# Kernel optimization log

Measured on AMD Instinct MI355X. Metric: run time of the kernel, lower is better.

Reference implementation:

```python
import jax, jax.numpy as jnp
import numpy as np

N = 20000      # CG beads
F = 78         # n_atom_basis (forced by reshape(-1,78) + Linear(n_atom_basis,39))
NRBF = 20
CUTOFF = 21.0
L = 3          # num_conv
DEG = 16
EH = N * DEG // 2
EPS = 1e-15


def silu(x):
    return x * jax.nn.sigmoid(x)


def setup_inputs() -> dict:
    key = jax.random.key(0)
    ks = jax.random.split(key, 22)
    cg_xyz = jax.random.normal(ks[0], (N, 3), jnp.float32) * 10.0
    half = jax.random.randint(ks[1], (EH, 2), 0, N)
    # symmetric (already-directed) edge list -> make_directed is a no-op
    CG_nbr_list = jnp.concatenate([half, half[:, ::-1]], axis=0)
    H = jax.random.normal(ks[2], (N, F), jnp.float32)
    mapping = jax.random.randint(ks[3], (N,), 0, N)  # unused by forward
    s = 0.05
    p = lambda k, shape: jax.random.normal(k, shape, jnp.float32) * s
    return {
        'cg_xyz': cg_xyz, 'CG_nbr_list': CG_nbr_list, 'mapping': mapping, 'H': H,
        # message blocks (stacked over L layers): inv_dense (F->F->4F) + dist_embed dense (NRBF->4F)
        'msg_w1': p(ks[4], (L, F, F)),   'msg_b1': jnp.zeros((L, F)),
        'msg_w2': p(ks[5], (L, F, 4 * F)), 'msg_b2': jnp.zeros((L, 4 * F)),
        'rbf_w':  p(ks[6], (L, NRBF, 4 * F)), 'rbf_b': jnp.zeros((L, 4 * F)),
        # update blocks: U, V linear maps (no bias) + s_dense (2F->F->3F)
        'upd_wu': p(ks[7], (L, F, F)), 'upd_wv': p(ks[8], (L, F, F)),
        'upd_w1': p(ks[9], (L, 2 * F, F)), 'upd_b1': jnp.zeros((L, F)),
        'upd_w2': p(ks[10], (L, F, 3 * F)), 'upd_b2': jnp.zeros((L, 3 * F)),
        # final dense head: ReLU -> Linear(78,39) -> ReLU -> Linear(39,39)
        'dense_w1': p(ks[11], (F, 39)), 'dense_b1': jnp.zeros((39,)),
        'dense_w2': p(ks[12], (39, 39)), 'dense_b2': jnp.zeros((39,)),
    }


def reference(cg_xyz, CG_nbr_list, mapping, H,
              msg_w1, msg_b1, msg_w2, msg_b2, rbf_w, rbf_b,
              upd_wu, upd_wv, upd_w1, upd_b1, upd_w2, upd_b2,
              dense_w1, dense_b1, dense_w2, dense_b2):
    n_nodes = H.shape[0]
    i_idx = CG_nbr_list[:, 0]
    j_idx = CG_nbr_list[:, 1]
    # edge geometry (shared across layers)
    r_ij = cg_xyz[j_idx] - cg_xyz[i_idx]                      # (E,3)
    dist = jnp.sqrt((r_ij ** 2 + EPS).sum(-1))                # (E,)
    unit = r_ij / dist[:, None]
    n = jnp.arange(1, NRBF + 1, dtype=cg_xyz.dtype)
    rbf = jnp.sin(n * jnp.pi * dist[:, None] / CUTOFF) / dist[:, None]   # (E,NRBF)
    env = jnp.where(dist < CUTOFF, 0.5 * (jnp.cos(jnp.pi * dist / CUTOFF) + 1.0), 0.0)

    V = jnp.zeros((n_nodes, H.shape[1], 3), H.dtype)          # (N,F,3)
    for l in range(L):
        # ---- EquiMessageCross ----
        phi = silu(H @ msg_w1[l] + msg_b1[l]) @ msg_w2[l] + msg_b2[l]     # (N,4F)
        w_s = (rbf @ rbf_w[l] + rbf_b[l]) * env[:, None]                  # (E,4F)
        inv = phi[j_idx] * w_s                                            # (E,4F)
        s0, s1, s2, s3 = jnp.split(inv, 4, axis=-1)                       # each (E,F)
        vj = V[j_idx]                                                     # (E,F,3)
        vi = V[i_idx]
        dv = (s2[..., None] * unit[:, None, :]
              + s1[..., None] * vj
              + s3[..., None] * jnp.cross(vi, vj, axis=-1))               # (E,F,3)
        H = H + jax.ops.segment_sum(s0, i_idx, num_segments=n_nodes)
        V = V + jax.ops.segment_sum(dv, i_idx, num_segments=n_nodes)
        # ---- UpdateBlock (PaiNN) ----
        u_v = jnp.einsum('nfc,fg->ngc', V, upd_wu[l])
        v_v = jnp.einsum('nfc,fg->ngc', V, upd_wv[l])
        v_norm = jnp.sqrt((v_v ** 2).sum(-1) + EPS)                       # (N,F)
        a = silu(jnp.concatenate([H, v_norm], -1) @ upd_w1[l] + upd_b1[l]) @ upd_w2[l] + upd_b2[l]
        a_vv, a_sv, a_ss = jnp.split(a, 3, axis=-1)
        H = H + a_sv * (u_v * v_v).sum(-1) + a_ss
        V = V + a_vv[..., None] * u_v

    Vs = V.sum(-1).reshape(-1, 78)                                        # (N,78)
    out = jax.nn.relu(Vs)
    out = jax.nn.relu(out @ dense_w1 + dense_b1) @ dense_w2 + dense_b2    # (N,39)
    return H, out.reshape(-1, 13, 3)
```

## Files before the change

### kernel.cpp

```cpp
#include <hip/hip_runtime.h>
#include <hip/hip_bf16.h>
#include <cmath>

#define N_NODES 20000
#define FF 78
#define F3 234
#define F4 312
#define NRBF 20
#define CUTOFF 21.0f
#define NL 3
#define PI_F 3.14159265358979323846f
#define EPS_F 1e-15f
#define REC_STRIDE 24
#define CHUNK 64
#define UV_RN 16

__global__ void k_init(const float* __restrict__ Hin, float* __restrict__ Hcur,
                       float* __restrict__ VA, uint2* __restrict__ VbfU,
                       int* __restrict__ counts, int* __restrict__ cursor)
{
    int idx = blockIdx.x * blockDim.x + threadIdx.x;
    int stride = gridDim.x * blockDim.x;
    for (int i = idx; i < N_NODES * F3; i += stride) {
        VA[i] = 0.f;
        if (i < N_NODES * FF) Hcur[i] = Hin[i];
        if (i < N_NODES * 78) VbfU[i] = make_uint2(0u, 0u);
        if (i < N_NODES) { counts[i] = 0; cursor[i] = 0; }
    }
}

__global__ void k_geo(const float* __restrict__ xyz, const int* __restrict__ nbr,
                      float4* __restrict__ geo, int* __restrict__ counts, int E)
{
    int e = blockIdx.x * blockDim.x + threadIdx.x;
    if (e >= E) return;
    int i = nbr[2 * e], j = nbr[2 * e + 1];
    float rx = xyz[3 * j]     - xyz[3 * i];
    float ry = xyz[3 * j + 1] - xyz[3 * i + 1];
    float rz = xyz[3 * j + 2] - xyz[3 * i + 2];
    float d = sqrtf(rx * rx + ry * ry + rz * rz + 3.0f * EPS_F);
    geo[e] = make_float4(rx / d, ry / d, rz / d, d);
    if (d < CUTOFF) atomicAdd(&counts[i], 1);
}

__global__ __launch_bounds__(1024)
void k_scan(const int* __restrict__ counts, int* __restrict__ row_start, int n)
{
    __shared__ int s[1024];
    const int t = threadIdx.x;
    constexpr int PER = 20;
    const int base = t * PER;
    int loc[PER];
    int sum = 0;
    #pragma unroll
    for (int q = 0; q < PER; ++q) {
        int idx = base + q;
        int v = (idx < n) ? counts[idx] : 0;
        loc[q] = sum;
        sum += v;
    }
    s[t] = sum;
    __syncthreads();
    for (int off = 1; off < 1024; off <<= 1) {
        int add = (t >= off) ? s[t - off] : 0;
        __syncthreads();
        s[t] += add;
        __syncthreads();
    }
    const int excl = (t > 0) ? s[t - 1] : 0;
    #pragma unroll
    for (int q = 0; q < PER; ++q) {
        int idx = base + q;
        if (idx <= n) row_start[idx] = excl + loc[q];
    }
}

__global__ void k_fill(const float4* __restrict__ geo, const int* __restrict__ nbr,
                       const int* __restrict__ row_start, int* __restrict__ cursor,
                       int* __restrict__ edge_idx, int E)
{
    int e = blockIdx.x * blockDim.x + threadIdx.x;
    if (e >= E) return;
    if (geo[e].w < CUTOFF) {
        int i = nbr[2 * e];
        int pos = row_start[i] + atomicAdd(&cursor[i], 1);
        edge_idx[pos] = e;
    }
}

__global__ void k_edgerec(const float4* __restrict__ geo, const int* __restrict__ edge_idx,
                          const int* __restrict__ nbr, const int* __restrict__ row_start,
                          float* __restrict__ rec, int* __restrict__ jl, int E)
{
    int p = blockIdx.x * blockDim.x + threadIdx.x;
    int total = row_start[N_NODES];
    if (p >= total) return;
    int eidx = edge_idx[p];
    float4 g = geo[eidx];
    float d = g.w;
    float env = 0.5f * (cosf(PI_F * d / CUTOFF) + 1.0f);
    float* r = rec + (size_t)p * REC_STRIDE;
    #pragma unroll
    for (int k = 0; k < NRBF; ++k)
        r[k] = env * sinf((float)(k + 1) * (PI_F / CUTOFF) * d) / d;
    r[20] = env;
    r[21] = g.x; r[22] = g.y; r[23] = g.z;
    jl[p] = nbr[2 * eidx + 1];
}

template<int K1T, int K2T, int NC2, int CS2, int BF16OUT>
__global__ void k_mlp2(const float* __restrict__ X1, const float* __restrict__ X2,
                       const float* __restrict__ w1, const float* __restrict__ b1,
                       const float* __restrict__ w2, const float* __restrict__ b2,
                       void* __restrict__ Yv, int nrows)
{
    constexpr int R = 32;
    constexpr int K = K1T + K2T;
    __shared__ float sX[K * R];
    __shared__ float s2[78 * 33];
    const int r0 = blockIdx.x * R;
    const int tid = threadIdx.y * 78 + threadIdx.x;
    for (int idx = tid; idx < R * K; idx += 312) {
        int r = idx / K, k = idx - r * K;
        int row = r0 + r;
        float v = 0.f;
        if (row < nrows) {
            if constexpr (K2T == 0) v = X1[(size_t)row * K1T + k];
            else v = (k < K1T) ? X1[(size_t)row * K1T + k] : X2[(size_t)row * K2T + (k - K1T)];
        }
        sX[k * R + r] = v;
    }
    __syncthreads();
    const int rg = threadIdx.y * 8;
    {
        const int c = threadIdx.x;
        float acc[8];
        #pragma unroll
        for (int q = 0; q < 8; ++q) acc[q] = 0.f;
        for (int k = 0; k < K; ++k) {
            const float w = w1[k * 78 + c];
            #pragma unroll
            for (int q = 0; q < 8; ++q) acc[q] = fmaf(w, sX[k * R + rg + q], acc[q]);
        }
        const float bb = b1[c];
        #pragma unroll
        for (int q = 0; q < 8; ++q) {
            float y = acc[q] + bb;
            y = y / (1.f + expf(-y));
            s2[c * 33 + rg + q] = y;
        }
    }
    __syncthreads();
    {
        const int c0 = threadIdx.x * CS2;
        float acc[8][CS2];
        #pragma unroll
        for (int q = 0; q < 8; ++q)
            #pragma unroll
            for (int cc = 0; cc < CS2; ++cc) acc[q][cc] = 0.f;
        for (int k = 0; k < 78; ++k) {
            float xv[8];
            #pragma unroll
            for (int q = 0; q < 8; ++q) xv[q] = s2[k * 33 + rg + q];
            float wv[CS2];
            #pragma unroll
            for (int cc = 0; cc < CS2; ++cc) wv[cc] = w2[(size_t)k * NC2 + c0 + cc];
            #pragma unroll
            for (int q = 0; q < 8; ++q)
                #pragma unroll
                for (int cc = 0; cc < CS2; ++cc) acc[q][cc] = fmaf(xv[q], wv[cc], acc[q][cc]);
        }
        #pragma unroll
        for (int q = 0; q < 8; ++q) {
            int row = r0 + rg + q;
            if (row < nrows) {
                if constexpr (BF16OUT && CS2 == 4) {
                    union { __hip_bfloat16 hh[4]; uint2 u; } pk;
                    #pragma unroll
                    for (int cc = 0; cc < 4; ++cc)
                        pk.hh[cc] = __float2bfloat16(acc[q][cc] + b2[c0 + cc]);
                    *(uint2*)&((__hip_bfloat16*)Yv)[(size_t)row * NC2 + c0] = pk.u;
                } else {
                    #pragma unroll
                    for (int cc = 0; cc < CS2; ++cc)
                        ((float*)Yv)[(size_t)row * NC2 + c0 + cc] = acc[q][cc] + b2[c0 + cc];
                }
            }
        }
    }
}

#define COMP_W(E_, W_, UX_, UY_, UZ_) do {                                          \
    const float4* r4_ = (const float4*)(rec + (size_t)(E_) * REC_STRIDE);           \
    const float4 q0=r4_[0], q1=r4_[1], q2=r4_[2], q3=r4_[3], q4=r4_[4], q5=r4_[5];  \
    float p0 = q0.x*wcol[0], p1 = q0.y*wcol[1], p2 = q0.z*wcol[2], p3 = q0.w*wcol[3]; \
    p0 = fmaf(q1.x, wcol[4],  p0);  p1 = fmaf(q1.y, wcol[5],  p1);                  \
    p2 = fmaf(q1.z, wcol[6],  p2);  p3 = fmaf(q1.w, wcol[7],  p3);                  \
    p0 = fmaf(q2.x, wcol[8],  p0);  p1 = fmaf(q2.y, wcol[9],  p1);                  \
    p2 = fmaf(q2.z, wcol[10], p2);  p3 = fmaf(q2.w, wcol[11], p3);                  \
    p0 = fmaf(q3.x, wcol[12], p0);  p1 = fmaf(q3.y, wcol[13], p1);                  \
    p2 = fmaf(q3.z, wcol[14], p2);  p3 = fmaf(q3.w, wcol[15], p3);                  \
    p0 = fmaf(q4.x, wcol[16], p0);  p1 = fmaf(q4.y, wcol[17], p1);                  \
    p2 = fmaf(q4.z, wcol[18], p2);  p3 = fmaf(q4.w, wcol[19], p3);                  \
    W_ = fmaf(wb, q5.x, (p0 + p1) + (p2 + p3));                                     \
    UX_ = q5.y; UY_ = q5.z; UZ_ = q5.w;                                             \
} while (0)

__global__ __launch_bounds__(320)
void k_message(const __hip_bfloat16* __restrict__ phi, const float* __restrict__ Vold,
               const __hip_bfloat16* __restrict__ Vbf,
               float* __restrict__ Vnew, float* __restrict__ Hcur,
               const float* __restrict__ rec, const int* __restrict__ jl,
               const int* __restrict__ row_start,
               const float* __restrict__ rbfw, const float* __restrict__ rbfb)
{
    const int i = blockIdx.x;
    const int t = threadIdx.x;
    const int tt = (t < 312) ? t : 156;
    const int cch = (tt < 78) ? tt + 78 : (tt < 156) ? tt + 156
                  : (tt < 234) ? tt - 156 : tt - 78;
    const int fv  = (tt < 78) ? tt : (tt < 156) ? tt - 78 : 0;
    const bool needvj = (tt < 156);
    const float sun = (tt >= 234) ? 1.f : 0.f;
    const float svj = needvj ? 1.f : 0.f;

    __shared__ float s_acc[3 * F3];
    __shared__ int s_j[CHUNK];

    const unsigned short* __restrict__ phiu = (const unsigned short*)phi;
    const unsigned short* __restrict__ vbfu = (const unsigned short*)Vbf;

    float wcol[NRBF];
    const float wb = rbfb[cch];
    #pragma unroll
    for (int k = 0; k < NRBF; ++k) wcol[k] = rbfw[k * F4 + cch];

    const int e0 = row_start[i], e1 = row_start[i + 1];
    float accH = 0.f, a0 = 0.f, a1 = 0.f, a2 = 0.f;

    float vix = 0.f, viy = 0.f, viz = 0.f;
    if (t >= 78 && t < 156) {
        const unsigned vb = (unsigned)i * F3 + (unsigned)fv * 3;
        vix = Vold[vb]; viy = Vold[vb + 1]; viz = Vold[vb + 2];
    }

    for (int base = e0; base < e1; base += CHUNK) {
        const int len = (e1 - base < CHUNK) ? (e1 - base) : CHUNK;
        if (t < len) s_j[t] = jl[base + t];
        __syncthreads();

        int jA = s_j[0];
        unsigned pfA = (unsigned)phiu[(size_t)jA * F4 + cch];
        uint2 vqA = make_uint2(0u, 0u);
        if (needvj) vqA = *(const uint2*)(vbfu + ((size_t)jA * F4 + 4u * fv));
        const int m1 = (1 < len) ? 1 : 0;
        int jB = s_j[m1];
        unsigned pfB = (unsigned)phiu[(size_t)jB * F4 + cch];
        uint2 vqB = make_uint2(0u, 0u);
        if (needvj) vqB = *(const uint2*)(vbfu + ((size_t)jB * F4 + 4u * fv));
        float wA, uxA, uyA, uzA;
        COMP_W(base, wA, uxA, uyA, uzA);

        for (int m = 0; m < len; ++m) {
            const int mw = (m + 1 < len) ? m + 1 : 0;
            const int m2 = (m + 2 < len) ? m + 2 : 0;
            float wN, uxN, uyN, uzN;
            COMP_W(base + mw, wN, uxN, uyN, uzN);
            const int jC = s_j[m2];
            const unsigned pfC = (unsigned)phiu[(size_t)jC * F4 + cch];
            uint2 vqC = make_uint2(0u, 0u);
            if (needvj) vqC = *(const uint2*)(vbfu + ((size_t)jC * F4 + 4u * fv));

            const float pv  = __uint_as_float(pfA << 16) * wA;
            const float vj0 = __uint_as_float(vqA.x << 16);
            const float vj1 = __uint_as_float(vqA.x & 0xffff0000u);
            const float vj2 = __uint_as_float(vqA.y << 16);
            a0 = fmaf(pv, fmaf(svj, vj0, sun * uxA), a0);
            a1 = fmaf(pv, fmaf(svj, vj1, sun * uyA), a1);
            a2 = fmaf(pv, fmaf(svj, vj2, sun * uzA), a2);
            accH += pv;

            pfA = pfB; vqA = vqB;
            wA = wN; uxA = uxN; uyA = uyN; uzA = uzN;
            pfB = pfC; vqB = vqC;
        }
        __syncthreads();
    }

    if (t >= 78 && t < 156) {
        const float m0 = a0, m1c = a1, m2c = a2;
        a0 = viy * m2c - viz * m1c;
        a1 = viz * m0  - vix * m2c;
        a2 = vix * m1c - viy * m0;
    }

    if (t < 78) {
        s_acc[3*tt] = a0; s_acc[3*tt+1] = a1; s_acc[3*tt+2] = a2;
    } else if (t < 156) {
        const int f = tt - 78;
        s_acc[F3 + 3*f] = a0; s_acc[F3 + 3*f+1] = a1; s_acc[F3 + 3*f+2] = a2;
    } else if (t >= 234 && t < 312) {
        const int f = tt - 234;
        s_acc[2*F3 + 3*f] = a0; s_acc[2*F3 + 3*f+1] = a1; s_acc[2*F3 + 3*f+2] = a2;
    }
    __syncthreads();
    if (t >= 156 && t < 234) Hcur[(unsigned)(i * FF + (t - 156))] += accH;
    for (int k = t; k < F3; k += 320)
        Vnew[(unsigned)(i * F3 + k)] = Vold[(unsigned)(i * F3 + k)]
            + s_acc[k] + s_acc[F3 + k] + s_acc[2*F3 + k];
}

__global__ __launch_bounds__(256)
void k_upd_uv(const float* __restrict__ V, const float* __restrict__ wu, const float* __restrict__ wv,
              float* __restrict__ u_v, float* __restrict__ v_v, float* __restrict__ vnorm)
{
    const int n0 = blockIdx.x * UV_RN;
    const int t = threadIdx.x;
    __shared__ float sV[UV_RN][240];
    for (int idx = t; idx < F3 * UV_RN; idx += 256) {
        int n = idx / F3, k = idx - n * F3;
        sV[n][k] = V[(size_t)(n0 + n) * F3 + k];
    }
    __syncthreads();
    float au[UV_RN], av[UV_RN];
    #pragma unroll
    for (int n = 0; n < UV_RN; ++n) { au[n] = 0.f; av[n] = 0.f; }
    if (t < F3) {
        const int g = t / 3, c = t - g * 3;
        for (int f = 0; f < FF; ++f) {
            const float wuv = wu[f * FF + g];
            const float wvv = wv[f * FF + g];
            const int kk = f * 3 + c;
            #pragma unroll
            for (int n = 0; n < UV_RN; ++n) {
                const float x = sV[n][kk];
                au[n] = fmaf(x, wuv, au[n]);
                av[n] = fmaf(x, wvv, av[n]);
            }
        }
        #pragma unroll
        for (int n = 0; n < UV_RN; ++n) {
            u_v[(size_t)(n0 + n) * F3 + t] = au[n];
            v_v[(size_t)(n0 + n) * F3 + t] = av[n];
        }
    }
    __syncthreads();
    if (t < F3) {
        #pragma unroll
        for (int n = 0; n < UV_RN; ++n) sV[n][t] = av[n];
    }
    __syncthreads();
    for (int idx = t; idx < FF * UV_RN; idx += 256) {
        int n = idx / FF, g = idx - n * FF;
        float a = sV[n][3*g], b = sV[n][3*g+1], c = sV[n][3*g+2];
        vnorm[(size_t)(n0 + n) * FF + g] = sqrtf(a * a + b * b + c * c + EPS_F);
    }
}

__global__ void k_upd_apply(const float* __restrict__ H, float* __restrict__ Hout,
                            float* __restrict__ V, __hip_bfloat16* __restrict__ Vbf,
                            const float* __restrict__ u_v, const float* __restrict__ v_v,
                            const float* __restrict__ a)
{
    int idx = blockIdx.x * blockDim.x + threadIdx.x;
    if (idx >= N_NODES * FF) return;
    int n = idx / FF, g = idx - n * FF;
    size_t b3 = (size_t)n * F3 + g * 3;
    float u0 = u_v[b3], u1 = u_v[b3+1], u2 = u_v[b3+2];
    float v0 = v_v[b3], v1 = v_v[b3+1], v2 = v_v[b3+2];
    float dot = u0*v0 + u1*v1 + u2*v2;
    size_t ab = (size_t)n * F3;
    float avv = a[ab + g], asv = a[ab + FF + g], ass = a[ab + 2*FF + g];
    Hout[idx] = H[idx] + asv * dot + ass;
    float nv0 = V[b3]   + avv * u0;
    float nv1 = V[b3+1] + avv * u1;
    float nv2 = V[b3+2] + avv * u2;
    V[b3] = nv0; V[b3+1] = nv1; V[b3+2] = nv2;
    union { __hip_bfloat16 hh[4]; uint2 u; } pk;
    pk.hh[0] = __float2bfloat16(nv0);
    pk.hh[1] = __float2bfloat16(nv1);
    pk.hh[2] = __float2bfloat16(nv2);
    pk.hh[3] = __float2bfloat16(0.f);
    *(uint2*)&Vbf[(size_t)n * F4 + g * 4] = pk.u;
}

__global__ __launch_bounds__(128)
void k_decode(const float* __restrict__ V, const float* __restrict__ w1, const float* __restrict__ b1,
              const float* __restrict__ w2, const float* __restrict__ b2, float* __restrict__ out)
{
    const int n = blockIdx.x, t = threadIdx.x;
    __shared__ float sx[FF];
    __shared__ float sh[39];
    if (t < FF) {
        size_t b = (size_t)n * F3 + t * 3;
        float x = V[b] + V[b+1] + V[b+2];
        sx[t] = fmaxf(x, 0.f);
    }
    __syncthreads();
    if (t < 39) {
        float h = b1[t];
        for (int g = 0; g < FF; ++g) h += sx[g] * w1[g * 39 + t];
        sh[t] = fmaxf(h, 0.f);
    }
    __syncthreads();
    if (t < 39) {
        float o = b2[t];
        for (int m = 0; m < 39; ++m) o += sh[m] * w2[m * 39 + t];
        out[(size_t)n * 39 + t] = o;
    }
}

extern "C" void kernel_launch(void* const* d_in, const int* in_sizes, int n_in,
                              void* d_out, int out_size, void* d_ws, size_t ws_size,
                              hipStream_t stream)
{
    const float* xyz    = (const float*)d_in[0];
    const int*   nbr    = (const int*)  d_in[1];
    const float* Hin    = (const float*)d_in[3];
    const float* msg_w1 = (const float*)d_in[4];
    const float* msg_b1 = (const float*)d_in[5];
    const float* msg_w2 = (const float*)d_in[6];
    const float* msg_b2 = (const float*)d_in[7];
    const float* rbf_w  = (const float*)d_in[8];
    const float* rbf_b  = (const float*)d_in[9];
    const float* upd_wu = (const float*)d_in[10];
    const float* upd_wv = (const float*)d_in[11];
    const float* upd_w1 = (const float*)d_in[12];
    const float* upd_b1 = (const float*)d_in[13];
    const float* upd_w2 = (const float*)d_in[14];
    const float* upd_b2 = (const float*)d_in[15];
    const float* dw1    = (const float*)d_in[16];
    const float* db1    = (const float*)d_in[17];
    const float* dw2    = (const float*)d_in[18];
    const float* db2    = (const float*)d_in[19];
    const int E = in_sizes[1] / 2;
    const int ECAP = E / 2 + E / 25;

    float* ws = (float*)d_ws;
    size_t off = 0;
    float* Hcur  = ws + off; off += (size_t)N_NODES * FF;
    float* VA    = ws + off; off += (size_t)N_NODES * F3;
    float* VB    = ws + off; off += (size_t)N_NODES * F3;
    __hip_bfloat16* phi = (__hip_bfloat16*)(ws + off); off += (size_t)N_NODES * F4 / 2;
    __hip_bfloat16* Vbf = (__hip_bfloat16*)(ws + off); off += (size_t)N_NODES * F4 / 2;
    float* u_v   = ws + off; off += (size_t)N_NODES * F3;
    float* v_v   = ws + off; off += (size_t)N_NODES * F3;
    float* vnorm = ws + off; off += (size_t)N_NODES * FF;
    float* a_buf = ws + off;
    float4* geo  = (float4*)a_buf;
    off += (size_t)N_NODES * F3;
    float* rec   = ws + off; off += (size_t)ECAP * REC_STRIDE;
    int* ibase     = (int*)(ws + off);
    int* row_start = ibase;
    int* counts    = row_start + (N_NODES + 1);
    int* cursor    = counts + N_NODES;
    int* edge_idx  = cursor + N_NODES;
    int* jl        = edge_idx + ECAP;

    k_init<<<dim3((N_NODES * F3 + 255) / 256), dim3(256), 0, stream>>>(
        Hin, Hcur, VA, (uint2*)Vbf, counts, cursor);
    k_geo<<<dim3((E + 255) / 256), dim3(256), 0, stream>>>(xyz, nbr, geo, counts, E);
    k_scan<<<dim3(1), dim3(1024), 0, stream>>>(counts, row_start, N_NODES);
    k_fill<<<dim3((E + 255) / 256), dim3(256), 0, stream>>>(geo, nbr, row_start, cursor, edge_idx, E);
    k_edgerec<<<dim3((E + 255) / 256), dim3(256), 0, stream>>>(geo, edge_idx, nbr, row_start, rec, jl, E);

    float* dout = (float*)d_out;
    float* Vold = VA;
    float* Vnew = VB;
    for (int l = 0; l < NL; ++l) {
        k_mlp2<78, 0, 312, 4, 1><<<dim3(625), dim3(78, 4), 0, stream>>>(
            Hcur, nullptr, msg_w1 + (size_t)l * 78 * 78, msg_b1 + (size_t)l * 78,
            msg_w2 + (size_t)l * 78 * 312, msg_b2 + (size_t)l * 312, phi, N_NODES);
        k_message<<<dim3(N_NODES), dim3(320), 0, stream>>>(
            phi, Vold, Vbf, Vnew, Hcur, rec, jl, row_start,
            rbf_w + (size_t)l * NRBF * F4, rbf_b + (size_t)l * F4);
        k_upd_uv<<<dim3(N_NODES / UV_RN), dim3(256), 0, stream>>>(
            Vnew, upd_wu + (size_t)l * 78 * 78, upd_wv + (size_t)l * 78 * 78, u_v, v_v, vnorm);
        k_mlp2<78, 78, 234, 3, 0><<<dim3(625), dim3(78, 4), 0, stream>>>(
            Hcur, vnorm, upd_w1 + (size_t)l * 156 * 78, upd_b1 + (size_t)l * 78,
            upd_w2 + (size_t)l * 78 * 234, upd_b2 + (size_t)l * 234, a_buf, N_NODES);
        float* Hout = (l == NL - 1) ? dout : Hcur;
        k_upd_apply<<<dim3((N_NODES * FF + 255) / 256), dim3(256), 0, stream>>>(
            Hcur, Hout, Vnew, Vbf, u_v, v_v, a_buf);
        float* tmp = Vold; Vold = Vnew; Vnew = tmp;
    }

    k_decode<<<dim3(N_NODES), dim3(128), 0, stream>>>(Vold, dw1, db1, dw2, db2, dout + (size_t)N_NODES * FF);
}
```

Baseline: 792.3 us.

## Fuse update MLP with apply, merge edge fill/record, process two nodes per message block

The update-block MLP now writes its three output slices straight into the apply step (H and V update plus the bf16 copy of V), which removes the a_buf round trip and one launch per layer. k_fill now computes the edge record and neighbor index directly at its atomically assigned slot, which drops edge_idx and the separate k_edgerec launch. k_message handles two nodes per block, halving the grid and reusing the rbf weight columns loaded into registers. In exchange, the fused update kernel carries more register and shared-memory pressure, and the two-node loop serialises work inside each block.

Result: no change. 778.6 us (-1.7%).

```diff
diff --git a/kernel.cpp b/kernel.cpp
--- a/kernel.cpp
+++ b/kernel.cpp
@@ -77,35 +77,24 @@
 
 __global__ void k_fill(const float4* __restrict__ geo, const int* __restrict__ nbr,
                        const int* __restrict__ row_start, int* __restrict__ cursor,
-                       int* __restrict__ edge_idx, int E)
+                       float* __restrict__ rec, int* __restrict__ jl, int E)
 {
     int e = blockIdx.x * blockDim.x + threadIdx.x;
     if (e >= E) return;
-    if (geo[e].w < CUTOFF) {
+    float4 g = geo[e];
+    if (g.w < CUTOFF) {
         int i = nbr[2 * e];
         int pos = row_start[i] + atomicAdd(&cursor[i], 1);
-        edge_idx[pos] = e;
-    }
-}
-
-__global__ void k_edgerec(const float4* __restrict__ geo, const int* __restrict__ edge_idx,
-                          const int* __restrict__ nbr, const int* __restrict__ row_start,
-                          float* __restrict__ rec, int* __restrict__ jl, int E)
-{
-    int p = blockIdx.x * blockDim.x + threadIdx.x;
-    int total = row_start[N_NODES];
-    if (p >= total) return;
-    int eidx = edge_idx[p];
-    float4 g = geo[eidx];
-    float d = g.w;
-    float env = 0.5f * (cosf(PI_F * d / CUTOFF) + 1.0f);
-    float* r = rec + (size_t)p * REC_STRIDE;
-    #pragma unroll
-    for (int k = 0; k < NRBF; ++k)
-        r[k] = env * sinf((float)(k + 1) * (PI_F / CUTOFF) * d) / d;
-    r[20] = env;
-    r[21] = g.x; r[22] = g.y; r[23] = g.z;
-    jl[p] = nbr[2 * eidx + 1];
+        float d = g.w;
+        float env = 0.5f * (cosf(PI_F * d / CUTOFF) + 1.0f);
+        float* r = rec + (size_t)pos * REC_STRIDE;
+        #pragma unroll
+        for (int k = 0; k < NRBF; ++k)
+            r[k] = env * sinf((float)(k + 1) * (PI_F / CUTOFF) * d) / d;
+        r[20] = env;
+        r[21] = g.x; r[22] = g.y; r[23] = g.z;
+        jl[pos] = nbr[2 * e + 1];
+    }
 }
 
 template<int K1T, int K2T, int NC2, int CS2, int BF16OUT>
@@ -190,6 +179,87 @@
     }
 }
 
+__global__ __launch_bounds__(312)
+void k_updmlp_apply(const float* __restrict__ H, const float* __restrict__ vnorm,
+                    const float* __restrict__ w1, const float* __restrict__ b1,
+                    const float* __restrict__ w2, const float* __restrict__ b2,
+                    const float* __restrict__ u_v, const float* __restrict__ v_v,
+                    float* __restrict__ V, __hip_bfloat16* __restrict__ Vbf,
+                    float* __restrict__ Hout)
+{
+    constexpr int R = 32;
+    __shared__ float sX[156 * R];
+    __shared__ float s2[78 * 33];
+    const int r0 = blockIdx.x * R;
+    const int tid = threadIdx.y * 78 + threadIdx.x;
+    for (int idx = tid; idx < R * 156; idx += 312) {
+        int r = idx / 156, k = idx - r * 156;
+        int row = r0 + r;
+        sX[k * R + r] = (k < 78) ? H[(size_t)row * FF + k]
+                                 : vnorm[(size_t)row * FF + (k - 78)];
+    }
+    __syncthreads();
+    const int rg = threadIdx.y * 8;
+    const int c = threadIdx.x;
+    {
+        float acc[8];
+        #pragma unroll
+        for (int q = 0; q < 8; ++q) acc[q] = 0.f;
+        for (int k = 0; k < 156; ++k) {
+            const float w = w1[k * 78 + c];
+            #pragma unroll
+            for (int q = 0; q < 8; ++q) acc[q] = fmaf(w, sX[k * R + rg + q], acc[q]);
+        }
+        const float bb = b1[c];
+        #pragma unroll
+        for (int q = 0; q < 8; ++q) {
+            float y = acc[q] + bb;
+            s2[c * 33 + rg + q] = y / (1.f + expf(-y));
+        }
+    }
+    __syncthreads();
+    {
+        float a0[8], a1[8], a2[8];
+        #pragma unroll
+        for (int q = 0; q < 8; ++q) { a0[q] = 0.f; a1[q] = 0.f; a2[q] = 0.f; }
+        for (int k = 0; k < 78; ++k) {
+            float xv[8];
+            #pragma unroll
+            for (int q = 0; q < 8; ++q) xv[q] = s2[k * 33 + rg + q];
+            const float w0 = w2[k * F3 + c];
+            const float w1v = w2[k * F3 + 78 + c];
+            const float w2v = w2[k * F3 + 156 + c];
+            #pragma unroll
+            for (int q = 0; q < 8; ++q) {
+                a0[q] = fmaf(xv[q], w0, a0[q]);
+                a1[q] = fmaf(xv[q], w1v, a1[q]);
+                a2[q] = fmaf(xv[q], w2v, a2[q]);
+            }
+        }
+        const float bvv = b2[c], bsv = b2[78 + c], bss = b2[156 + c];
+        #pragma unroll
+        for (int q = 0; q < 8; ++q) {
+            const int row = r0 + rg + q;
+            const float avv = a0[q] + bvv, asv = a1[q] + bsv, ass = a2[q] + bss;
+            const size_t b3 = (size_t)row * F3 + c * 3;
+            const float u0 = u_v[b3], u1 = u_v[b3 + 1], u2 = u_v[b3 + 2];
+            const float v0 = v_v[b3], v1 = v_v[b3 + 1], v2 = v_v[b3 + 2];
+            const float dot = u0 * v0 + u1 * v1 + u2 * v2;
+            Hout[(size_t)row * FF + c] = sX[c * R + rg + q] + asv * dot + ass;
+            const float nv0 = V[b3]     + avv * u0;
+            const float nv1 = V[b3 + 1] + avv * u1;
+            const float nv2 = V[b3 + 2] + avv * u2;
+            V[b3] = nv0; V[b3 + 1] = nv1; V[b3 + 2] = nv2;
+            union { __hip_bfloat16 hh[4]; uint2 u; } pk;
+            pk.hh[0] = __float2bfloat16(nv0);
+            pk.hh[1] = __float2bfloat16(nv1);
+            pk.hh[2] = __float2bfloat16(nv2);
+            pk.hh[3] = __float2bfloat16(0.f);
+            *(uint2*)&Vbf[(size_t)row * F4 + c * 4] = pk.u;
+        }
+    }
+}
+
 #define COMP_W(E_, W_, UX_, UY_, UZ_) do {                                          \
     const float4* r4_ = (const float4*)(rec + (size_t)(E_) * REC_STRIDE);           \
     const float4 q0=r4_[0], q1=r4_[1], q2=r4_[2], q3=r4_[3], q4=r4_[4], q5=r4_[5];  \
@@ -214,7 +284,6 @@
                const int* __restrict__ row_start,
                const float* __restrict__ rbfw, const float* __restrict__ rbfb)
 {
-    const int i = blockIdx.x;
     const int t = threadIdx.x;
     const int tt = (t < 312) ? t : 156;
     const int cch = (tt < 78) ? tt + 78 : (tt < 156) ? tt + 156
@@ -235,79 +304,83 @@
     #pragma unroll
     for (int k = 0; k < NRBF; ++k) wcol[k] = rbfw[k * F4 + cch];
 
-    const int e0 = row_start[i], e1 = row_start[i + 1];
-    float accH = 0.f, a0 = 0.f, a1 = 0.f, a2 = 0.f;
-
-    float vix = 0.f, viy = 0.f, viz = 0.f;
-    if (t >= 78 && t < 156) {
-        const unsigned vb = (unsigned)i * F3 + (unsigned)fv * 3;
-        vix = Vold[vb]; viy = Vold[vb + 1]; viz = Vold[vb + 2];
-    }
-
-    for (int base = e0; base < e1; base += CHUNK) {
-        const int len = (e1 - base < CHUNK) ? (e1 - base) : CHUNK;
-        if (t < len) s_j[t] = jl[base + t];
+    for (int nn = 0; nn < 2; ++nn) {
+        const int i = blockIdx.x * 2 + nn;
+        const int e0 = row_start[i], e1 = row_start[i + 1];
+        float accH = 0.f, a0 = 0.f, a1 = 0.f, a2 = 0.f;
+
+        float vix = 0.f, viy = 0.f, viz = 0.f;
+        if (t >= 78 && t < 156) {
+            const unsigned vb = (unsigned)i * F3 + (unsigned)fv * 3;
+            vix = Vold[vb]; viy = Vold[vb + 1]; viz = Vold[vb + 2];
+        }
+
+        for (int base = e0; base < e1; base += CHUNK) {
+            const int len = (e1 - base < CHUNK) ? (e1 - base) : CHUNK;
+            if (t < len) s_j[t] = jl[base + t];
+            __syncthreads();
+
+            int jA = s_j[0];
+            unsigned pfA = (unsigned)phiu[(size_t)jA * F4 + cch];
+            uint2 vqA = make_uint2(0u, 0u);
+            if (needvj) vqA = *(const uint2*)(vbfu + ((size_t)jA * F4 + 4u * fv));
+            const int m1 = (1 < len) ? 1 : 0;
+            int jB = s_j[m1];
+            unsigned pfB = (unsigned)phiu[(size_t)jB * F4 + cch];
+            uint2 vqB = make_uint2(0u, 0u);
+            if (needvj) vqB = *(const uint2*)(vbfu + ((size_t)jB * F4 + 4u * fv));
+            float wA, uxA, uyA, uzA;
+            COMP_W(base, wA, uxA, uyA, uzA);
+
+            for (int m = 0; m < len; ++m) {
+                const int mw = (m + 1 < len) ? m + 1 : 0;
+                const int m2 = (m + 2 < len) ? m + 2 : 0;
+                float wN, uxN, uyN, uzN;
+                COMP_W(base + mw, wN, uxN, uyN, uzN);
+                const int jC = s_j[m2];
+                const unsigned pfC = (unsigned)phiu[(size_t)jC * F4 + cch];
+                uint2 vqC = make_uint2(0u, 0u);
+                if (needvj) vqC = *(const uint2*)(vbfu + ((size_t)jC * F4 + 4u * fv));
+
+                const float pv  = __uint_as_float(pfA << 16) * wA;
+                const float vj0 = __uint_as_float(vqA.x << 16);
+                const float vj1 = __uint_as_float(vqA.x & 0xffff0000u);
+                const float vj2 = __uint_as_float(vqA.y << 16);
+                a0 = fmaf(pv, fmaf(svj, vj0, sun * uxA), a0);
+                a1 = fmaf(pv, fmaf(svj, vj1, sun * uyA), a1);
+                a2 = fmaf(pv, fmaf(svj, vj2, sun * uzA), a2);
+                accH += pv;
+
+                pfA = pfB; vqA = vqB;
+                wA = wN; uxA = uxN; uyA = uyN; uzA = uzN;
+                pfB = pfC; vqB = vqC;
+            }
+            __syncthreads();
+        }
+
+        if (t >= 78 && t < 156) {
+            const float m0 = a0, m1c = a1, m2c = a2;
+            a0 = viy * m2c - viz * m1c;
+            a1 = viz * m0  - vix * m2c;
+            a2 = vix * m1c - viy * m0;
+        }
+
+        if (t < 78) {
+            s_acc[3*tt] = a0; s_acc[3*tt+1] = a1; s_acc[3*tt+2] = a2;
+        } else if (t < 156) {
+            const int f = tt - 78;
+            s_acc[F3 + 3*f] = a0; s_acc[F3 + 3*f+1] = a1; s_acc[F3 + 3*f+2] = a2;
+        } else if (t >= 234 && t < 312) {
+            const int f = tt - 234;
+            s_acc[2*F3 + 3*f] = a0; s_acc[2*F3 + 3*f+1] = a1; s_acc[2*F3 + 3*f+2] = a2;
+        }
         __syncthreads();
-
-        int jA = s_j[0];
-        unsigned pfA = (unsigned)phiu[(size_t)jA * F4 + cch];
-        uint2 vqA = make_uint2(0u, 0u);
-        if (needvj) vqA = *(const uint2*)(vbfu + ((size_t)jA * F4 + 4u * fv));
-        const int m1 = (1 < len) ? 1 : 0;
-        int jB = s_j[m1];
-        unsigned pfB = (unsigned)phiu[(size_t)jB * F4 + cch];
-        uint2 vqB = make_uint2(0u, 0u);
-        if (needvj) vqB = *(const uint2*)(vbfu + ((size_t)jB * F4 + 4u * fv));
-        float wA, uxA, uyA, uzA;
-        COMP_W(base, wA, uxA, uyA, uzA);
-
-        for (int m = 0; m < len; ++m) {
-            const int mw = (m + 1 < len) ? m + 1 : 0;
-            const int m2 = (m + 2 < len) ? m + 2 : 0;
-            float wN, uxN, uyN, uzN;
-            COMP_W(base + mw, wN, uxN, uyN, uzN);
-            const int jC = s_j[m2];
-            const unsigned pfC = (unsigned)phiu[(size_t)jC * F4 + cch];
-            uint2 vqC = make_uint2(0u, 0u);
-            if (needvj) vqC = *(const uint2*)(vbfu + ((size_t)jC * F4 + 4u * fv));
-
-            const float pv  = __uint_as_float(pfA << 16) * wA;
-            const float vj0 = __uint_as_float(vqA.x << 16);
-            const float vj1 = __uint_as_float(vqA.x & 0xffff0000u);
-            const float vj2 = __uint_as_float(vqA.y << 16);
-            a0 = fmaf(pv, fmaf(svj, vj0, sun * uxA), a0);
-            a1 = fmaf(pv, fmaf(svj, vj1, sun * uyA), a1);
-            a2 = fmaf(pv, fmaf(svj, vj2, sun * uzA), a2);
-            accH += pv;
-
-            pfA = pfB; vqA = vqB;
-            wA = wN; uxA = uxN; uyA = uyN; uzA = uzN;
-            pfB = pfC; vqB = vqC;
-        }
+        if (t >= 156 && t < 234) Hcur[(unsigned)(i * FF + (t - 156))] += accH;
+        for (int k = t; k < F3; k += 320)
+            Vnew[(unsigned)(i * F3 + k)] = Vold[(unsigned)(i * F3 + k)]
+                + s_acc[k] + s_acc[F3 + k] + s_acc[2*F3 + k];
         __syncthreads();
     }
-
-    if (t >= 78 && t < 156) {
-        const float m0 = a0, m1c = a1, m2c = a2;
-        a0 = viy * m2c - viz * m1c;
-        a1 = viz * m0  - vix * m2c;
-        a2 = vix * m1c - viy * m0;
-    }
-
-    if (t < 78) {
-        s_acc[3*tt] = a0; s_acc[3*tt+1] = a1; s_acc[3*tt+2] = a2;
-    } else if (t < 156) {
-        const int f = tt - 78;
-        s_acc[F3 + 3*f] = a0; s_acc[F3 + 3*f+1] = a1; s_acc[F3 + 3*f+2] = a2;
-    } else if (t >= 234 && t < 312) {
-        const int f = tt - 234;
-        s_acc[2*F3 + 3*f] = a0; s_acc[2*F3 + 3*f+1] = a1; s_acc[2*F3 + 3*f+2] = a2;
-    }
-    __syncthreads();
-    if (t >= 156 && t < 234) Hcur[(unsigned)(i * FF + (t - 156))] += accH;
-    for (int k = t; k < F3; k += 320)
-        Vnew[(unsigned)(i * F3 + k)] = Vold[(unsigned)(i * F3 + k)]
-            + s_acc[k] + s_acc[F3 + k] + s_acc[2*F3 + k];
 }
 
 __global__ __launch_bounds__(256)
@@ -355,33 +428,6 @@
         float a = sV[n][3*g], b = sV[n][3*g+1], c = sV[n][3*g+2];
         vnorm[(size_t)(n0 + n) * FF + g] = sqrtf(a * a + b * b + c * c + EPS_F);
     }
-}
-
-__global__ void k_upd_apply(const float* __restrict__ H, float* __restrict__ Hout,
-                            float* __restrict__ V, __hip_bfloat16* __restrict__ Vbf,
-                            const float* __restrict__ u_v, const float* __restrict__ v_v,
-                            const float* __restrict__ a)
-{
-    int idx = blockIdx.x * blockDim.x + threadIdx.x;
-    if (idx >= N_NODES * FF) return;
-    int n = idx / FF, g = idx - n * FF;
-    size_t b3 = (size_t)n * F3 + g * 3;
-    float u0 = u_v[b3], u1 = u_v[b3+1], u2 = u_v[b3+2];
-    float v0 = v_v[b3], v1 = v_v[b3+1], v2 = v_v[b3+2];
-    float dot = u0*v0 + u1*v1 + u2*v2;
-    size_t ab = (size_t)n * F3;
-    float avv = a[ab + g], asv = a[ab + FF + g], ass = a[ab + 2*FF + g];
-    Hout[idx] = H[idx] + asv * dot + ass;
-    float nv0 = V[b3]   + avv * u0;
-    float nv1 = V[b3+1] + avv * u1;
-    float nv2 = V[b3+2] + avv * u2;
-    V[b3] = nv0; V[b3+1] = nv1; V[b3+2] = nv2;
-    union { __hip_bfloat16 hh[4]; uint2 u; } pk;
-    pk.hh[0] = __float2bfloat16(nv0);
-    pk.hh[1] = __float2bfloat16(nv1);
-    pk.hh[2] = __float2bfloat16(nv2);
-    pk.hh[3] = __float2bfloat16(0.f);
-    *(uint2*)&Vbf[(size_t)n * F4 + g * 4] = pk.u;
 }
 
 __global__ __launch_bounds__(128)
@@ -446,23 +492,19 @@
     float* u_v   = ws + off; off += (size_t)N_NODES * F3;
     float* v_v   = ws + off; off += (size_t)N_NODES * F3;
     float* vnorm = ws + off; off += (size_t)N_NODES * FF;
-    float* a_buf = ws + off;
-    float4* geo  = (float4*)a_buf;
-    off += (size_t)N_NODES * F3;
+    float4* geo  = (float4*)(ws + off); off += (size_t)E * 4;
     float* rec   = ws + off; off += (size_t)ECAP * REC_STRIDE;
     int* ibase     = (int*)(ws + off);
     int* row_start = ibase;
     int* counts    = row_start + (N_NODES + 1);
     int* cursor    = counts + N_NODES;
-    int* edge_idx  = cursor + N_NODES;
-    int* jl        = edge_idx + ECAP;
+    int* jl        = cursor + N_NODES;
 
     k_init<<<dim3((N_NODES * F3 + 255) / 256), dim3(256), 0, stream>>>(
         Hin, Hcur, VA, (uint2*)Vbf, counts, cursor);
     k_geo<<<dim3((E + 255) / 256), dim3(256), 0, stream>>>(xyz, nbr, geo, counts, E);
     k_scan<<<dim3(1), dim3(1024), 0, stream>>>(counts, row_start, N_NODES);
-    k_fill<<<dim3((E + 255) / 256), dim3(256), 0, stream>>>(geo, nbr, row_start, cursor, edge_idx, E);
-    k_edgerec<<<dim3((E + 255) / 256), dim3(256), 0, stream>>>(geo, edge_idx, nbr, row_start, rec, jl, E);
+    k_fill<<<dim3((E + 255) / 256), dim3(256), 0, stream>>>(geo, nbr, row_start, cursor, rec, jl, E);
 
     float* dout = (float*)d_out;
     float* Vold = VA;
@@ -471,17 +513,16 @@
         k_mlp2<78, 0, 312, 4, 1><<<dim3(625), dim3(78, 4), 0, stream>>>(
             Hcur, nullptr, msg_w1 + (size_t)l * 78 * 78, msg_b1 + (size_t)l * 78,
             msg_w2 + (size_t)l * 78 * 312, msg_b2 + (size_t)l * 312, phi, N_NODES);
-        k_message<<<dim3(N_NODES), dim3(320), 0, stream>>>(
+        k_message<<<dim3(N_NODES / 2), dim3(320), 0, stream>>>(
             phi, Vold, Vbf, Vnew, Hcur, rec, jl, row_start,
             rbf_w + (size_t)l * NRBF * F4, rbf_b + (size_t)l * F4);
         k_upd_uv<<<dim3(N_NODES / UV_RN), dim3(256), 0, stream>>>(
             Vnew, upd_wu + (size_t)l * 78 * 78, upd_wv + (size_t)l * 78 * 78, u_v, v_v, vnorm);
-        k_mlp2<78, 78, 234, 3, 0><<<dim3(625), dim3(78, 4), 0, stream>>>(
+        float* Hout = (l == NL - 1) ? dout : Hcur;
+        k_updmlp_apply<<<dim3(625), dim3(78, 4), 0, stream>>>(
             Hcur, vnorm, upd_w1 + (size_t)l * 156 * 78, upd_b1 + (size_t)l * 78,
-            upd_w2 + (size_t)l * 78 * 234, upd_b2 + (size_t)l * 234, a_buf, N_NODES);
-        float* Hout = (l == NL - 1) ? dout : Hcur;
-        k_upd_apply<<<dim3((N_NODES * FF + 255) / 256), dim3(256), 0, stream>>>(
-            Hcur, Hout, Vnew, Vbf, u_v, v_v, a_buf);
+            upd_w2 + (size_t)l * 78 * 234, upd_b2 + (size_t)l * 234,
+            u_v, v_v, Vnew, Vbf, Hout);
         float* tmp = Vold; Vold = Vnew; Vnew = tmp;
     }
 
```
